# Kernel tuning notes

Hardware: AMD Instinct MI355X
Metric: run time of the kernel (lower is better)

Reference implementation:

```python
import jax, jax.numpy as jnp
import numpy as np

EPS = 1e-12  # torch F.normalize default eps


def conv1x1(x, w, b):
    # x: [N,C,H,W], w: [O,C], b: [O]
    return jnp.einsum('nchw,oc->nohw', x, w) + b[None, :, None, None]


def forward_sa(f1, f2, cw1, cb1, cw2, cb2):
    c1 = conv1x1(f1, cw1, cb1)  # [N,1,H,W]
    c2 = conv1x1(f2, cw2, cb2)
    n, _, h, w = c1.shape
    c1 = jax.nn.softmax(c1.reshape(n, 1, h * w), axis=-1).reshape(n, 1, h, w)
    c2 = jax.nn.softmax(c2.reshape(n, 1, h * w), axis=-1).reshape(n, 1, h, w)
    return c1 * f1, c2 * f2


def l2_normalize_ch(x):
    # F.normalize(x): L2 over channel dim (dim=1), norm clamped to eps
    n = jnp.sqrt(jnp.sum(x * x, axis=1, keepdims=True))
    return x / jnp.maximum(n, EPS)


def forward_ca(f1, f2, pw1, pb1, pw2, pb2):
    N, C, H, W = f1.shape
    HW = H * W
    f1_cl = conv1x1(f1, pw1, pb1).reshape(N, -1, HW)  # [N,Cl,HW]
    f2_cl = conv1x1(f2, pw2, pb2).reshape(N, -1, HW)
    # A = f2_cl^T @ f1_cl : [N,HW,HW]
    A_c = jnp.tanh(jnp.einsum('nci,ncj->nij', f2_cl, f1_cl))
    f1_v = f1.reshape(N, C, HW)
    f2_v = f2.reshape(N, C, HW)
    # f1_hat = f1_v @ A_c^T ; f2_hat = f2_v @ A_c
    f1_hat = jnp.einsum('ncj,nij->nci', f1_v, A_c).reshape(N, C, H, W)
    f2_hat = jnp.einsum('ncj,nji->nci', f2_v, A_c).reshape(N, C, H, W)
    return l2_normalize_ch(f1_hat), l2_normalize_ch(f2_hat)


def setup_inputs() -> dict:
    key = jax.random.key(0)
    ks = jax.random.split(key, 10)
    N, C, H, W = 8, 256, 32, 32
    Cl = C // 16
    return {
        'f1': jax.random.normal(ks[0], (N, C, H, W), jnp.float32),
        'f2': jax.random.normal(ks[1], (N, C, H, W), jnp.float32),
        'pw1': jax.random.normal(ks[2], (Cl, C), jnp.float32) * 0.05,
        'pb1': jax.random.normal(ks[3], (Cl,), jnp.float32) * 0.05,
        'pw2': jax.random.normal(ks[4], (Cl, C), jnp.float32) * 0.05,
        'pb2': jax.random.normal(ks[5], (Cl,), jnp.float32) * 0.05,
        'cw1': jax.random.normal(ks[6], (1, C), jnp.float32) * 0.05,
        'cb1': jax.random.normal(ks[7], (1,), jnp.float32) * 0.05,
        'cw2': jax.random.normal(ks[8], (1, C), jnp.float32) * 0.05,
        'cb2': jax.random.normal(ks[9], (1,), jnp.float32) * 0.05,
    }


def reference(f1, f2, pw1, pb1, pw2, pb2, cw1, cb1, cw2, cb2):
    fp1, fp2 = f1, f2
    for i in range(5):
        s1, s2 = forward_sa(fp1, fp2, cw1, cb1, cw2, cb2)
        h1, h2 = forward_ca(s1, s2, pw1, pb1, pw2, pb2)
        if i < 4:
            fp1 = jax.nn.relu(h1 + fp1)
            fp2 = jax.nn.relu(h2 + fp2)
    return h1, h2, s1, s2
```

## Files before the change

kernel.cpp:

```cpp
#include <hip/hip_runtime.h>
#include <cstdint>
#include <cstddef>

#define N_  8
#define C_  256
#define HW_ 1024
#define CL_ 16
#define SZ_ (N_*C_*HW_)
#define WSCALE_ 4096.0f

typedef __attribute__((ext_vector_type(8))) _Float16 half8;
typedef __attribute__((ext_vector_type(4))) float f32x4;

static __device__ __forceinline__ float tanh_fast(float x){
  x = fminf(fmaxf(x, -15.f), 15.f);
  float e = __expf(2.f * x);
  return (e - 1.f) / (e + 1.f);
}

static __device__ __forceinline__ unsigned short f2h(float x){
  _Float16 h = (_Float16)x;
  return *(unsigned short*)&h;
}

static __device__ __forceinline__ void combine16(
    const float* __restrict__ mpart, const float* __restrict__ spart,
    int base, float& m, float& rl)
{
  m = -1e30f;
  #pragma unroll
  for (int k = 0; k < 16; ++k) m = fmaxf(m, mpart[base * 16 + k]);
  float s = 0.f;
  #pragma unroll
  for (int k = 0; k < 16; ++k) s += spart[base * 16 + k] * __expf(mpart[base * 16 + k] - m);
  rl = 1.f / s;
}

#define GLD16(g, l) __builtin_amdgcn_global_load_lds( \
    (const __attribute__((address_space(1))) void*)(g), \
    (__attribute__((address_space(3))) void*)(l), 16, 0, 0)

__global__ __launch_bounds__(256) void k_cvt(
    const float* __restrict__ f1, const float* __restrict__ f2,
    _Float16* __restrict__ o1, _Float16* __restrict__ o2)
{
  const int side = blockIdx.y;
  const size_t o = ((size_t)blockIdx.x * 256 + threadIdx.x) * 8;
  const float* __restrict__ f = side ? f2 : f1;
  _Float16* __restrict__ oo = side ? o2 : o1;
  const float4 v0 = *(const float4*)&f[o];
  const float4 v1 = *(const float4*)&f[o + 4];
  half8 r;
  r[0] = (_Float16)v0.x; r[1] = (_Float16)v0.y; r[2] = (_Float16)v0.z; r[3] = (_Float16)v0.w;
  r[4] = (_Float16)v1.x; r[5] = (_Float16)v1.y; r[6] = (_Float16)v1.z; r[7] = (_Float16)v1.w;
  *(half8*)&oo[o] = r;
}

__global__ __launch_bounds__(256) void k_sa_dot(
    const float* __restrict__ fp1, const float* __restrict__ fp2,
    const float* __restrict__ cw1, const float* __restrict__ cw2,
    const float* __restrict__ pw1, const float* __restrict__ pw2,
    float* __restrict__ cval, float* __restrict__ pdot,
    float* __restrict__ mpart, float* __restrict__ spart)
{
  const int n = blockIdx.z, side = blockIdx.y, hw0 = blockIdx.x * 64;
  const int t = threadIdx.x, hwl = t & 63, cg = t >> 6;
  const float* __restrict__ pw = side ? pw2 : pw1;
  const float* __restrict__ cw = side ? cw2 : cw1;
  const float* __restrict__ f  = (side ? fp2 : fp1) + (size_t)n * C_ * HW_ + hw0 + hwl;
  const int cb = __builtin_amdgcn_readfirstlane(cg * 64);

  float acc[17];
  #pragma unroll
  for (int l = 0; l < 17; ++l) acc[l] = 0.f;

  for (int cc = 0; cc < 64; ++cc){
    const int c = cb + cc;
    const float v = f[(size_t)c * HW_];
    acc[16] += v * cw[c];
    #pragma unroll
    for (int l = 0; l < 16; ++l) acc[l] += v * pw[l * C_ + c];
  }

  __shared__ float red[17][4][64];
  #pragma unroll
  for (int l = 0; l < 17; ++l) red[l][cg][hwl] = acc[l];
  __syncthreads();

  if (t < 64){
    const int base = n * 2 + side;
    float xc = 0.f;
    #pragma unroll
    for (int l = 0; l < 17; ++l){
      const float s = red[l][0][t] + red[l][1][t] + red[l][2][t] + red[l][3][t];
      if (l < 16) pdot[((size_t)base * CL_ + l) * HW_ + hw0 + t] = s;
      else      { cval[(size_t)base * HW_ + hw0 + t] = s; xc = s; }
    }
    float mb = xc;
    #pragma unroll
    for (int off = 32; off; off >>= 1) mb = fmaxf(mb, __shfl_xor(mb, off));
    float e = __expf(xc - mb);
    #pragma unroll
    for (int off = 32; off; off >>= 1) e += __shfl_xor(e, off);
    if (t == 0){
      mpart[base * 16 + blockIdx.x] = mb;
      spart[base * 16 + blockIdx.x] = e;
    }
  }
}

__global__ __launch_bounds__(256) void k_corr(
    const float* __restrict__ cval, const float* __restrict__ pdot,
    const float* __restrict__ pb1, const float* __restrict__ pb2,
    const float* __restrict__ mpart, const float* __restrict__ spart,
    unsigned short* __restrict__ Abf, unsigned short* __restrict__ Atbf)
{
  const int n = blockIdx.z, i0 = blockIdx.y * 64, j0 = blockIdx.x * 64;
  const int b1 = n * 2, b2 = n * 2 + 1;
  __align__(16) __shared__ float s2[CL_][64];
  __align__(16) __shared__ float s1[CL_][64];
  __shared__ unsigned short at_s[64][68];
  const int t = threadIdx.x;
  const int lr = t >> 4, lc = (t & 15) * 4;

  float m1, rl1, m2, rl2;
  combine16(mpart, spart, b1, m1, rl1);
  combine16(mpart, spart, b2, m2, rl2);

  {
    const float bias2 = pb2[lr];
    const float4 c2 = *(const float4*)&cval[(size_t)b2 * HW_ + i0 + lc];
    const float4 p2 = *(const float4*)&pdot[((size_t)b2 * CL_ + lr) * HW_ + i0 + lc];
    s2[lr][lc + 0] = __expf(c2.x - m2) * rl2 * p2.x + bias2;
    s2[lr][lc + 1] = __expf(c2.y - m2) * rl2 * p2.y + bias2;
    s2[lr][lc + 2] = __expf(c2.z - m2) * rl2 * p2.z + bias2;
    s2[lr][lc + 3] = __expf(c2.w - m2) * rl2 * p2.w + bias2;

    const float bias1 = pb1[lr];
    const float4 c1 = *(const float4*)&cval[(size_t)b1 * HW_ + j0 + lc];
    const float4 p1 = *(const float4*)&pdot[((size_t)b1 * CL_ + lr) * HW_ + j0 + lc];
    s1[lr][lc + 0] = __expf(c1.x - m1) * rl1 * p1.x + bias1;
    s1[lr][lc + 1] = __expf(c1.y - m1) * rl1 * p1.y + bias1;
    s1[lr][lc + 2] = __expf(c1.z - m1) * rl1 * p1.z + bias1;
    s1[lr][lc + 3] = __expf(c1.w - m1) * rl1 * p1.w + bias1;
  }
  __syncthreads();

  const int ti = t >> 4, tj = t & 15;
  float acc[4][4];
  #pragma unroll
  for (int a = 0; a < 4; ++a)
    #pragma unroll
    for (int b = 0; b < 4; ++b) acc[a][b] = 0.f;

  #pragma unroll
  for (int l = 0; l < CL_; ++l){
    const float4 a4 = *(const float4*)&s2[l][ti * 4];
    const float4 b4 = *(const float4*)&s1[l][tj * 4];
    const float av[4] = {a4.x, a4.y, a4.z, a4.w};
    const float bv[4] = {b4.x, b4.y, b4.z, b4.w};
    #pragma unroll
    for (int a = 0; a < 4; ++a)
      #pragma unroll
      for (int b = 0; b < 4; ++b) acc[a][b] += av[a] * bv[b];
  }

  float tf[4][4];
  #pragma unroll
  for (int a = 0; a < 4; ++a)
    #pragma unroll
    for (int b = 0; b < 4; ++b) tf[a][b] = tanh_fast(acc[a][b]);

  float w1j[4], w2i[4];
  #pragma unroll
  for (int b = 0; b < 4; ++b)
    w1j[b] = WSCALE_ * __expf(cval[(size_t)b1 * HW_ + j0 + tj * 4 + b] - m1) * rl1;
  #pragma unroll
  for (int a = 0; a < 4; ++a)
    w2i[a] = WSCALE_ * __expf(cval[(size_t)b2 * HW_ + i0 + ti * 4 + a] - m2) * rl2;

  unsigned short* __restrict__ An  = Abf  + ((size_t)n << 20);
  unsigned short* __restrict__ Atn = Atbf + ((size_t)n << 20);
  #pragma unroll
  for (int a = 0; a < 4; ++a){
    ushort4 va;
    va.x = f2h(tf[a][0] * w1j[0]); va.y = f2h(tf[a][1] * w1j[1]);
    va.z = f2h(tf[a][2] * w1j[2]); va.w = f2h(tf[a][3] * w1j[3]);
    *(ushort4*)&An[(size_t)(i0 + ti * 4 + a) * HW_ + j0 + tj * 4] = va;
  }
  #pragma unroll
  for (int b = 0; b < 4; ++b){
    ushort4 vb;
    vb.x = f2h(tf[0][b] * w2i[0]); vb.y = f2h(tf[1][b] * w2i[1]);
    vb.z = f2h(tf[2][b] * w2i[2]); vb.w = f2h(tf[3][b] * w2i[3]);
    *(ushort4*)&at_s[tj * 4 + b][ti * 4] = vb;
  }
  __syncthreads();
  #pragma unroll
  for (int rep = 0; rep < 2; ++rep){
    const int idx = t + rep * 256;
    const int r = idx >> 3, q = (idx & 7) * 8;
    const ushort4 lo = *(const ushort4*)&at_s[r][q];
    const ushort4 hi = *(const ushort4*)&at_s[r][q + 4];
    *(ushort4*)&Atn[(size_t)(j0 + r) * HW_ + i0 + q] = lo;
    *(ushort4*)&Atn[(size_t)(j0 + r) * HW_ + i0 + q + 4] = hi;
  }
}

__global__ __launch_bounds__(512, 2) void k_gemm_fused(
    const _Float16* __restrict__ fhc1, const _Float16* __restrict__ fhc2,
    const unsigned short* __restrict__ Abf, const unsigned short* __restrict__ Atbf,
    const float* __restrict__ fpin1, const float* __restrict__ fpin2,
    float* __restrict__ fpo1, float* __restrict__ fpo2,
    _Float16* __restrict__ fhn1, _Float16* __restrict__ fhn2,
    const float* __restrict__ pw1, const float* __restrict__ pw2,
    const float* __restrict__ cw1, const float* __restrict__ cw2,
    float* __restrict__ cval, float* __restrict__ pdot,
    float* __restrict__ mpart, float* __restrict__ spart,
    float* __restrict__ out, int last)
{
  const int n = blockIdx.z, g = blockIdx.y, i0 = blockIdx.x * 64;
  const unsigned short* __restrict__ X =
      (const unsigned short*)((g ? fhc2 : fhc1) + (size_t)n * C_ * HW_);
  const unsigned short* __restrict__ B = (g ? Atbf : Abf) + ((size_t)n << 20);

  __shared__ __align__(16) unsigned char pool[81920];

  const int t = threadIdx.x, w = t >> 6, l = t & 63;
  const int wr = w >> 1, wc = w & 1;

  f32x4 acc[4][2];
  #pragma unroll
  for (int fm = 0; fm < 4; ++fm)
    #pragma unroll
    for (int fn = 0; fn < 2; ++fn)
      acc[fm][fn] = (f32x4){0.f, 0.f, 0.f, 0.f};

  auto stage = [&](int buf, int k0){
    unsigned short* Xsb = (unsigned short*)(pool + buf * 32768);
    unsigned short* Bsb = (unsigned short*)(pool + 65536 + buf * 8192);
    #pragma unroll
    for (int s = 0; s < 4; ++s){
      const int q = (w * 4 + s) * 64 + l;
      const int row = q >> 3;
      const int kc = (q & 7) ^ (row & 7);
      GLD16(X + (size_t)row * HW_ + k0 + kc * 8, &Xsb[(w * 4 + s) * 512]);
    }
    {
      const int q = w * 64 + l;
      const int row = q >> 3;
      const int kc = (q & 7) ^ (row & 7);
      GLD16(B + (size_t)(i0 + row) * HW_ + k0 + kc * 8, &Bsb[w * 512]);
    }
  };

  stage(0, 0);
  stage(1, 64);
  for (int kt = 0; kt < 16; ++kt){
    if (kt < 15) { asm volatile("s_waitcnt vmcnt(5)" ::: "memory"); }
    else         { asm volatile("s_waitcnt vmcnt(0)" ::: "memory"); }
    __builtin_amdgcn_sched_barrier(0);
    __builtin_amdgcn_s_barrier();
    const int cur = kt & 1;
    const unsigned short* Xsb = (const unsigned short*)(pool + cur * 32768);
    const unsigned short* Bsb = (const unsigned short*)(pool + 65536 + cur * 8192);
    #pragma unroll
    for (int ks = 0; ks < 2; ++ks){
      half8 a[4], bb[2];
      #pragma unroll
      for (int fm = 0; fm < 4; ++fm){
        const int row = wr * 64 + fm * 16 + (l & 15);
        const int kc = (ks * 4 + (l >> 4)) ^ (row & 7);
        a[fm] = *(const half8*)&Xsb[row * 64 + kc * 8];
      }
      #pragma unroll
      for (int fn = 0; fn < 2; ++fn){
        const int row = wc * 32 + fn * 16 + (l & 15);
        const int kc = (ks * 4 + (l >> 4)) ^ (row & 7);
        bb[fn] = *(const half8*)&Bsb[row * 64 + kc * 8];
      }
      #pragma unroll
      for (int fm = 0; fm < 4; ++fm)
        #pragma unroll
        for (int fn = 0; fn < 2; ++fn)
          acc[fm][fn] = __builtin_amdgcn_mfma_f32_16x16x32_f16(a[fm], bb[fn], acc[fm][fn], 0, 0, 0);
    }
    asm volatile("s_waitcnt lgkmcnt(0)" ::: "memory");
    __builtin_amdgcn_sched_barrier(0);
    __builtin_amdgcn_s_barrier();
    __builtin_amdgcn_sched_barrier(0);
    if (kt < 14) stage(cur, (kt + 2) * 64);
  }

  float* pwT   = (float*)pool;
  float* redp  = (float*)(pool + 32768);
  float* ssred = (float*)(pool + 65536);
  float* rinvp = (float*)(pool + 66560);

  float ss0 = 0.f, ss1 = 0.f;
  #pragma unroll
  for (int fm = 0; fm < 4; ++fm)
    #pragma unroll
    for (int r = 0; r < 4; ++r){
      ss0 += acc[fm][0][r] * acc[fm][0][r];
      ss1 += acc[fm][1][r] * acc[fm][1][r];
    }
  ss0 += __shfl_xor(ss0, 16); ss0 += __shfl_xor(ss0, 32);
  ss1 += __shfl_xor(ss1, 16); ss1 += __shfl_xor(ss1, 32);
  if (l < 16){
    ssred[wr * 64 + wc * 32 + l]      = ss0;
    ssred[wr * 64 + wc * 32 + 16 + l] = ss1;
  }

  if (!last){
    const float* __restrict__ pw = g ? pw2 : pw1;
    const float* __restrict__ cw = g ? cw2 : cw1;
    {
      const int idx = t * 8;
      const int lq = idx >> 8, c = idx & 255;
      const float4 p0 = *(const float4*)&pw[lq * C_ + c];
      const float4 p1 = *(const float4*)&pw[lq * C_ + c + 4];
      pwT[(c + 0) * 20 + lq] = p0.x; pwT[(c + 1) * 20 + lq] = p0.y;
      pwT[(c + 2) * 20 + lq] = p0.z; pwT[(c + 3) * 20 + lq] = p0.w;
      pwT[(c + 4) * 20 + lq] = p1.x; pwT[(c + 5) * 20 + lq] = p1.y;
      pwT[(c + 6) * 20 + lq] = p1.z; pwT[(c + 7) * 20 + lq] = p1.w;
    }
    if (t < 32){
      const float4 c0 = *(const float4*)&cw[t * 8];
      const float4 c1 = *(const float4*)&cw[t * 8 + 4];
      pwT[(t * 8 + 0) * 20 + 16] = c0.x; pwT[(t * 8 + 1) * 20 + 16] = c0.y;
      pwT[(t * 8 + 2) * 20 + 16] = c0.z; pwT[(t * 8 + 3) * 20 + 16] = c0.w;
      pwT[(t * 8 + 4) * 20 + 16] = c1.x; pwT[(t * 8 + 5) * 20 + 16] = c1.y;
      pwT[(t * 8 + 6) * 20 + 16] = c1.z; pwT[(t * 8 + 7) * 20 + 16] = c1.w;
    }
  }
  __syncthreads();
  if (t < 64){
    const float s = ssred[t] + ssred[64 + t] + ssred[128 + t] + ssred[192 + t];
    rinvp[t] = 1.f / fmaxf(sqrtf(s), 1e-12f);
  }
  __syncthreads();
  const float ri[2] = { rinvp[wc * 32 + (l & 15)], rinvp[wc * 32 + 16 + (l & 15)] };

  const float* __restrict__ fpin = (g ? fpin2 : fpin1) + (size_t)n * C_ * HW_;
  float* __restrict__ fpo  = (g ? fpo2 : fpo1) + (size_t)n * C_ * HW_;
  _Float16* __restrict__ fhn = (g ? fhn2 : fhn1) + (size_t)n * C_ * HW_;
  float* __restrict__ outp = out + (size_t)g * SZ_ + (size_t)n * C_ * HW_;
  const int rbase = (l >> 4) * 4, col = l & 15;
  const int baseio = n * 2 + g;

  if (!last){
    float sacc[2][17];
    #pragma unroll
    for (int fn = 0; fn < 2; ++fn)
      #pragma unroll
      for (int lq = 0; lq < 17; ++lq) sacc[fn][lq] = 0.f;

    #pragma unroll
    for (int fm = 0; fm < 4; ++fm)
      #pragma unroll
      for (int r = 0; r < 4; ++r){
        const int c = wr * 64 + fm * 16 + rbase + r;
        float prow[17];
        #pragma unroll
        for (int q4 = 0; q4 < 4; ++q4){
          const float4 pv = *(const float4*)&pwT[c * 20 + q4 * 4];
          prow[q4 * 4 + 0] = pv.x; prow[q4 * 4 + 1] = pv.y;
          prow[q4 * 4 + 2] = pv.z; prow[q4 * 4 + 3] = pv.w;
        }
        prow[16] = pwT[c * 20 + 16];
        #pragma unroll
        for (int fn = 0; fn < 2; ++fn){
          const size_t base = (size_t)c * HW_ + i0 + wc * 32 + fn * 16 + col;
          const float h = acc[fm][fn][r] * ri[fn];
          const float fv = fpin[base] + h;
          const float rv = fv > 0.f ? fv : 0.f;
          fpo[base] = rv;
          fhn[base] = (_Float16)rv;
          #pragma unroll
          for (int lq = 0; lq < 17; ++lq) sacc[fn][lq] += rv * prow[lq];
        }
      }

    #pragma unroll
    for (int fn = 0; fn < 2; ++fn)
      #pragma unroll
      for (int lq = 0; lq < 17; ++lq){
        float v = sacc[fn][lq];
        v += __shfl_xor(v, 16);
        v += __shfl_xor(v, 32);
        sacc[fn][lq] = v;
      }
    if (l < 16){
      #pragma unroll
      for (int fn = 0; fn < 2; ++fn)
        #pragma unroll
        for (int lq = 0; lq < 17; ++lq)
          redp[(((wr * 2 + wc) * 2 + fn) * 17 + lq) * 16 + l] = sacc[fn][lq];
    }
    __syncthreads();
    if (t < 64){
      const int wcx = t >> 5, fnx = (t >> 4) & 1, colx = t & 15;
      float xc = 0.f;
      #pragma unroll
      for (int lq = 0; lq < 17; ++lq){
        float s = 0.f;
        #pragma unroll
        for (int wrx = 0; wrx < 4; ++wrx)
          s += redp[(((wrx * 2 + wcx) * 2 + fnx) * 17 + lq) * 16 + colx];
        if (lq < 16) pdot[((size_t)baseio * CL_ + lq) * HW_ + i0 + t] = s;
        else       { cval[(size_t)baseio * HW_ + i0 + t] = s; xc = s; }
      }
      float mb = xc;
      #pragma unroll
      for (int off = 32; off; off >>= 1) mb = fmaxf(mb, __shfl_xor(mb, off));
      float e = __expf(xc - mb);
      #pragma unroll
      for (int off = 32; off; off >>= 1) e += __shfl_xor(e, off);
      if (t == 0){
        mpart[baseio * 16 + (i0 >> 6)] = mb;
        spart[baseio * 16 + (i0 >> 6)] = e;
      }
    }
  } else {
    #pragma unroll
    for (int fm = 0; fm < 4; ++fm)
      #pragma unroll
      for (int fn = 0; fn < 2; ++fn){
        const size_t base = (size_t)(wr * 64 + fm * 16 + rbase) * HW_ + i0 + wc * 32 + fn * 16 + col;
        #pragma unroll
        for (int r = 0; r < 4; ++r)
          outp[base + (size_t)r * HW_] = acc[fm][fn][r] * ri[fn];
      }
  }
}

__global__ __launch_bounds__(256) void k_s_out(
    const float* __restrict__ fp1, const float* __restrict__ fp2,
    const float* __restrict__ cval,
    const float* __restrict__ mpart, const float* __restrict__ spart,
    float* __restrict__ out)
{
  const int side = blockIdx.y;
  const size_t fo = ((size_t)blockIdx.x * 256 + threadIdx.x) * 4;
  const float* __restrict__ f = side ? fp2 : fp1;
  const int n  = (int)(fo >> 18);
  const int hw = (int)(fo & (HW_ - 1));
  const int base = n * 2 + side;
  float m, rl;
  combine16(mpart, spart, base, m, rl);
  const float4 c = *(const float4*)&cval[(size_t)base * HW_ + hw];
  const float4 v = *(const float4*)&f[fo];
  float4 r;
  r.x = v.x * (__expf(c.x - m) * rl);
  r.y = v.y * (__expf(c.y - m) * rl);
  r.z = v.z * (__expf(c.z - m) * rl);
  r.w = v.w * (__expf(c.w - m) * rl);
  *(float4*)&out[(size_t)(2 + side) * SZ_ + fo] = r;
}

extern "C" void kernel_launch(void* const* d_in, const int* in_sizes, int n_in,
                              void* d_out, int out_size, void* d_ws, size_t ws_size,
                              hipStream_t stream)
{
  const float* f1  = (const float*)d_in[0];
  const float* f2  = (const float*)d_in[1];
  const float* pw1 = (const float*)d_in[2];
  const float* pb1 = (const float*)d_in[3];
  const float* pw2 = (const float*)d_in[4];
  const float* pb2 = (const float*)d_in[5];
  const float* cw1 = (const float*)d_in[6];
  const float* cw2 = (const float*)d_in[8];
  float* out = (float*)d_out;
  float* ws  = (float*)d_ws;

  float* cval  = ws;
  float* pdot  = cval + N_ * 2 * HW_;
  float* mpart = pdot + N_ * 2 * CL_ * HW_;
  float* spart = mpart + 512;
  float* fp1   = spart + 512;
  float* fp2   = fp1 + SZ_;
  _Float16* fhA1 = (_Float16*)(fp2 + SZ_);
  _Float16* fhA2 = fhA1 + SZ_;
  _Float16* fhB1 = fhA2 + SZ_;
  _Float16* fhB2 = fhB1 + SZ_;
  unsigned short* Abf  = (unsigned short*)(fhB2 + SZ_);
  unsigned short* Atbf = Abf + ((size_t)N_ << 20);

  k_cvt<<<dim3(SZ_ / 8 / 256, 2), 256, 0, stream>>>(f1, f2, fhA1, fhA2);
  k_sa_dot<<<dim3(16, 2, 8), 256, 0, stream>>>(f1, f2, cw1, cw2, pw1, pw2,
                                               cval, pdot, mpart, spart);

  for (int it = 0; it < 5; ++it){
    const float* cur1 = (it == 0) ? f1 : fp1;
    const float* cur2 = (it == 0) ? f2 : fp2;
    const _Float16* fhc1 = (it & 1) ? fhB1 : fhA1;
    const _Float16* fhc2 = (it & 1) ? fhB2 : fhA2;
    _Float16* fhn1 = (it & 1) ? fhA1 : fhB1;
    _Float16* fhn2 = (it & 1) ? fhA2 : fhB2;

    k_corr<<<dim3(16, 16, 8), 256, 0, stream>>>(cval, pdot, pb1, pb2, mpart, spart, Abf, Atbf);
    if (it == 4)
      k_s_out<<<dim3(SZ_ / 4 / 256, 2), 256, 0, stream>>>(cur1, cur2, cval, mpart, spart, out);
    k_gemm_fused<<<dim3(16, 2, 8), 512, 0, stream>>>(fhc1, fhc2, Abf, Atbf,
                                                     cur1, cur2, fp1, fp2, fhn1, fhn2,
                                                     pw1, pw2, cw1, cw2,
                                                     cval, pdot, mpart, spart,
                                                     out, (it == 4) ? 1 : 0);
  }
}
```

Baseline: 243.1 us.

## Use triple-buffered K=32 pipeline in fused GEMM and fold fp16 conversion into sa_dot

The fused GEMM now stages K in 32-wide slices with a three-deep LDS ring instead of 64-wide double buffering. This shrinks shared memory to 60KB, and launch bounds are raised so more blocks can fit per CU and latency is hidden better. The separate fp32-to-fp16 conversion kernel is removed; k_sa_dot writes the half copy while it reads the inputs, saving one launch and one extra read pass. The trade-offs are more barriers per K step, and k_sa_dot now does scalar 2-byte strided stores. The grid is only 256 blocks, so the higher occupancy may be unused.

```diff
diff --git a/kernel.cpp b/kernel.cpp
--- a/kernel.cpp
+++ b/kernel.cpp
@@ -40,34 +40,22 @@
     (const __attribute__((address_space(1))) void*)(g), \
     (__attribute__((address_space(3))) void*)(l), 16, 0, 0)
 
-__global__ __launch_bounds__(256) void k_cvt(
-    const float* __restrict__ f1, const float* __restrict__ f2,
-    _Float16* __restrict__ o1, _Float16* __restrict__ o2)
-{
-  const int side = blockIdx.y;
-  const size_t o = ((size_t)blockIdx.x * 256 + threadIdx.x) * 8;
-  const float* __restrict__ f = side ? f2 : f1;
-  _Float16* __restrict__ oo = side ? o2 : o1;
-  const float4 v0 = *(const float4*)&f[o];
-  const float4 v1 = *(const float4*)&f[o + 4];
-  half8 r;
-  r[0] = (_Float16)v0.x; r[1] = (_Float16)v0.y; r[2] = (_Float16)v0.z; r[3] = (_Float16)v0.w;
-  r[4] = (_Float16)v1.x; r[5] = (_Float16)v1.y; r[6] = (_Float16)v1.z; r[7] = (_Float16)v1.w;
-  *(half8*)&oo[o] = r;
-}
+#define WAITV(N) asm volatile("s_waitcnt vmcnt(" #N ")" ::: "memory")
 
 __global__ __launch_bounds__(256) void k_sa_dot(
     const float* __restrict__ fp1, const float* __restrict__ fp2,
     const float* __restrict__ cw1, const float* __restrict__ cw2,
     const float* __restrict__ pw1, const float* __restrict__ pw2,
     float* __restrict__ cval, float* __restrict__ pdot,
-    float* __restrict__ mpart, float* __restrict__ spart)
+    float* __restrict__ mpart, float* __restrict__ spart,
+    _Float16* __restrict__ fh1, _Float16* __restrict__ fh2)
 {
   const int n = blockIdx.z, side = blockIdx.y, hw0 = blockIdx.x * 64;
   const int t = threadIdx.x, hwl = t & 63, cg = t >> 6;
   const float* __restrict__ pw = side ? pw2 : pw1;
   const float* __restrict__ cw = side ? cw2 : cw1;
   const float* __restrict__ f  = (side ? fp2 : fp1) + (size_t)n * C_ * HW_ + hw0 + hwl;
+  _Float16* __restrict__ fh = (side ? fh2 : fh1) + (size_t)n * C_ * HW_ + hw0 + hwl;
   const int cb = __builtin_amdgcn_readfirstlane(cg * 64);
 
   float acc[17];
@@ -77,6 +65,7 @@
   for (int cc = 0; cc < 64; ++cc){
     const int c = cb + cc;
     const float v = f[(size_t)c * HW_];
+    fh[(size_t)c * HW_] = (_Float16)v;
     acc[16] += v * cw[c];
     #pragma unroll
     for (int l = 0; l < 16; ++l) acc[l] += v * pw[l * C_ + c];
@@ -207,7 +196,7 @@
   }
 }
 
-__global__ __launch_bounds__(512, 2) void k_gemm_fused(
+__global__ __launch_bounds__(512, 4) void k_gemm_fused(
     const _Float16* __restrict__ fhc1, const _Float16* __restrict__ fhc2,
     const unsigned short* __restrict__ Abf, const unsigned short* __restrict__ Atbf,
     const float* __restrict__ fpin1, const float* __restrict__ fpin2,
@@ -224,7 +213,7 @@
       (const unsigned short*)((g ? fhc2 : fhc1) + (size_t)n * C_ * HW_);
   const unsigned short* __restrict__ B = (g ? Atbf : Abf) + ((size_t)n << 20);
 
-  __shared__ __align__(16) unsigned char pool[81920];
+  __shared__ __align__(16) unsigned char pool[61440];
 
   const int t = threadIdx.x, w = t >> 6, l = t & 63;
   const int wr = w >> 1, wc = w & 1;
@@ -237,65 +226,76 @@
       acc[fm][fn] = (f32x4){0.f, 0.f, 0.f, 0.f};
 
   auto stage = [&](int buf, int k0){
-    unsigned short* Xsb = (unsigned short*)(pool + buf * 32768);
-    unsigned short* Bsb = (unsigned short*)(pool + 65536 + buf * 8192);
-    #pragma unroll
-    for (int s = 0; s < 4; ++s){
-      const int q = (w * 4 + s) * 64 + l;
-      const int row = q >> 3;
-      const int kc = (q & 7) ^ (row & 7);
-      GLD16(X + (size_t)row * HW_ + k0 + kc * 8, &Xsb[(w * 4 + s) * 512]);
-    }
-    {
+    unsigned short* Xsb = (unsigned short*)(pool + buf * 16384);
+    #pragma unroll
+    for (int s = 0; s < 2; ++s){
+      const int q = (w * 2 + s) * 64 + l;
+      const int row = q >> 2;
+      const int kc = (q & 3) ^ (row & 3);
+      GLD16(X + (size_t)row * HW_ + k0 + kc * 8, &Xsb[(w * 2 + s) * 512]);
+    }
+    if (w < 4){
+      unsigned short* Bsb = (unsigned short*)(pool + 49152 + buf * 4096);
       const int q = w * 64 + l;
-      const int row = q >> 3;
-      const int kc = (q & 7) ^ (row & 7);
+      const int row = q >> 2;
+      const int kc = (q & 3) ^ (row & 3);
       GLD16(B + (size_t)(i0 + row) * HW_ + k0 + kc * 8, &Bsb[w * 512]);
     }
   };
 
   stage(0, 0);
-  stage(1, 64);
-  for (int kt = 0; kt < 16; ++kt){
-    if (kt < 15) { asm volatile("s_waitcnt vmcnt(5)" ::: "memory"); }
-    else         { asm volatile("s_waitcnt vmcnt(0)" ::: "memory"); }
+  stage(1, 32);
+  stage(2, 64);
+
+  int cur = 0;
+  for (int kt = 0; kt < 32; ++kt){
+    const int rem = (31 - kt) < 2 ? (31 - kt) : 2;
+    if (w < 4){
+      if (rem == 2)      WAITV(6);
+      else if (rem == 1) WAITV(3);
+      else               WAITV(0);
+    } else {
+      if (rem == 2)      WAITV(4);
+      else if (rem == 1) WAITV(2);
+      else               WAITV(0);
+    }
     __builtin_amdgcn_sched_barrier(0);
     __builtin_amdgcn_s_barrier();
-    const int cur = kt & 1;
-    const unsigned short* Xsb = (const unsigned short*)(pool + cur * 32768);
-    const unsigned short* Bsb = (const unsigned short*)(pool + 65536 + cur * 8192);
-    #pragma unroll
-    for (int ks = 0; ks < 2; ++ks){
-      half8 a[4], bb[2];
-      #pragma unroll
-      for (int fm = 0; fm < 4; ++fm){
-        const int row = wr * 64 + fm * 16 + (l & 15);
-        const int kc = (ks * 4 + (l >> 4)) ^ (row & 7);
-        a[fm] = *(const half8*)&Xsb[row * 64 + kc * 8];
-      }
-      #pragma unroll
-      for (int fn = 0; fn < 2; ++fn){
-        const int row = wc * 32 + fn * 16 + (l & 15);
-        const int kc = (ks * 4 + (l >> 4)) ^ (row & 7);
-        bb[fn] = *(const half8*)&Bsb[row * 64 + kc * 8];
-      }
-      #pragma unroll
-      for (int fm = 0; fm < 4; ++fm)
-        #pragma unroll
-        for (int fn = 0; fn < 2; ++fn)
-          acc[fm][fn] = __builtin_amdgcn_mfma_f32_16x16x32_f16(a[fm], bb[fn], acc[fm][fn], 0, 0, 0);
-    }
+
+    const unsigned short* Xsb = (const unsigned short*)(pool + cur * 16384);
+    const unsigned short* Bsb = (const unsigned short*)(pool + 49152 + cur * 4096);
+    half8 a[4], bb[2];
+    #pragma unroll
+    for (int fm = 0; fm < 4; ++fm){
+      const int row = wr * 64 + fm * 16 + (l & 15);
+      const int kc = (l >> 4) ^ (row & 3);
+      a[fm] = *(const half8*)&Xsb[row * 32 + kc * 8];
+    }
+    #pragma unroll
+    for (int fn = 0; fn < 2; ++fn){
+      const int row = wc * 32 + fn * 16 + (l & 15);
+      const int kc = (l >> 4) ^ (row & 3);
+      bb[fn] = *(const half8*)&Bsb[row * 32 + kc * 8];
+    }
+    #pragma unroll
+    for (int fm = 0; fm < 4; ++fm)
+      #pragma unroll
+      for (int fn = 0; fn < 2; ++fn)
+        acc[fm][fn] = __builtin_amdgcn_mfma_f32_16x16x32_f16(a[fm], bb[fn], acc[fm][fn], 0, 0, 0);
+
     asm volatile("s_waitcnt lgkmcnt(0)" ::: "memory");
     __builtin_amdgcn_sched_barrier(0);
     __builtin_amdgcn_s_barrier();
     __builtin_amdgcn_sched_barrier(0);
-    if (kt < 14) stage(cur, (kt + 2) * 64);
+
+    if (kt < 29) stage(cur, (kt + 3) * 32);
+    cur = (cur == 2) ? 0 : cur + 1;
   }
 
   float* pwT   = (float*)pool;
-  float* redp  = (float*)(pool + 32768);
-  float* ssred = (float*)(pool + 65536);
-  float* rinvp = (float*)(pool + 66560);
+  float* redp  = (float*)(pool + 20480);
+  float* ssred = (float*)(pool + 55296);
+  float* rinvp = (float*)(pool + 56320);
 
   float ss0 = 0.f, ss1 = 0.f;
   #pragma unroll
@@ -487,9 +487,8 @@
   unsigned short* Abf  = (unsigned short*)(fhB2 + SZ_);
   unsigned short* Atbf = Abf + ((size_t)N_ << 20);
 
-  k_cvt<<<dim3(SZ_ / 8 / 256, 2), 256, 0, stream>>>(f1, f2, fhA1, fhA2);
   k_sa_dot<<<dim3(16, 2, 8), 256, 0, stream>>>(f1, f2, cw1, cw2, pw1, pw2,
-                                               cval, pdot, mpart, spart);
+                                               cval, pdot, mpart, spart, fhA1, fhA2);
 
   for (int it = 0; it < 5; ++it){
     const float* cur1 = (it == 0) ? f1 : fp1;
```

Result: no change. 239.5 us (-1.5%).
